# Optimization experiments

Hardware: AMD Instinct MI355X
Metric: run time of the kernel (lower is better)

The kernel has to match this reference:

```python
import jax, jax.numpy as jnp
import numpy as np

D = 1024
H = 16
HD = D // H
FF = 4 * D

def layer_norm(x, g, b, eps=1e-5):
    mu = jnp.mean(x, axis=-1, keepdims=True)
    var = jnp.var(x, axis=-1, keepdims=True)
    return (x - mu) * jax.lax.rsqrt(var + eps) * g + b

def setup_inputs() -> dict:
    key = jax.random.key(0)
    ks = jax.random.split(key, 8)
    s = 0.02
    return {
        "x": jax.random.normal(ks[0], (2, 2048, D), jnp.float32),
        "ln1_g": jnp.ones((D,), jnp.float32),
        "ln1_b": jnp.zeros((D,), jnp.float32),
        "w_qkv": jax.random.normal(ks[1], (3 * D, D), jnp.float32) * s,
        "b_qkv": jnp.zeros((3 * D,), jnp.float32),
        "w_proj": jax.random.normal(ks[2], (D, D), jnp.float32) * s,
        "b_proj": jnp.zeros((D,), jnp.float32),
        "ln2_g": jnp.ones((D,), jnp.float32),
        "ln2_b": jnp.zeros((D,), jnp.float32),
        "w_fc1": jax.random.normal(ks[3], (FF, D), jnp.float32) * s,
        "b_fc1": jnp.zeros((FF,), jnp.float32),
        "w_fc2": jax.random.normal(ks[4], (D, FF), jnp.float32) * s,
        "b_fc2": jnp.zeros((D,), jnp.float32),
    }

def reference(x, ln1_g, ln1_b, w_qkv, b_qkv, w_proj, b_proj,
              ln2_g, ln2_b, w_fc1, b_fc1, w_fc2, b_fc2):
    B, N, C = x.shape
    scale = HD ** -0.5
    # --- attention branch (pre-norm) ---
    h = layer_norm(x, ln1_g, ln1_b)
    qkv = h @ w_qkv.T + b_qkv                      # [B,N,3D]
    qkv = qkv.reshape(B, N, 3, H, HD).transpose(2, 0, 3, 1, 4)
    q, k, v = qkv[0], qkv[1], qkv[2]               # [B,H,N,HD]
    attn = jnp.einsum('bhnd,bhmd->bhnm', q, k) * scale
    attn = jax.nn.softmax(attn, axis=-1)
    o = jnp.einsum('bhnm,bhmd->bhnd', attn, v)     # [B,H,N,HD]
    o = o.transpose(0, 2, 1, 3).reshape(B, N, C)
    x = x + (o @ w_proj.T + b_proj)
    # --- FFN branch (pre-norm) ---
    h = layer_norm(x, ln2_g, ln2_b)
    h = jax.nn.gelu(h @ w_fc1.T + b_fc1, approximate=False)
    x = x + (h @ w_fc2.T + b_fc2)
    return x
```

## Files before the change

### kernel.cpp

```cpp
#include <hip/hip_runtime.h>

typedef __attribute__((ext_vector_type(8))) short short8;
typedef __attribute__((ext_vector_type(4))) float f32x4;

static __device__ __forceinline__ unsigned short f2bf(float f){
  unsigned u = __float_as_uint(f);
  u += 0x7FFF + ((u >> 16) & 1);
  return (unsigned short)(u >> 16);
}

static __device__ __forceinline__ f32x4 MF(short8 a, short8 b, f32x4 c){
  return __builtin_amdgcn_mfma_f32_16x16x32_bf16(a, b, c, 0, 0, 0);
}

#define GL16(g, l) __builtin_amdgcn_global_load_lds( \
    (const __attribute__((address_space(1))) void*)(g), \
    (__attribute__((address_space(3))) void*)(l), 16, 0, 0)

#define SBAR { __builtin_amdgcn_sched_barrier(0); __builtin_amdgcn_s_barrier(); __builtin_amdgcn_sched_barrier(0); }

__global__ __launch_bounds__(256) void cvt_all(
    const float* __restrict__ a0, const float* __restrict__ a1,
    const float* __restrict__ a2, const float* __restrict__ a3,
    unsigned short* __restrict__ o0, unsigned short* __restrict__ o1,
    unsigned short* __restrict__ o2, unsigned short* __restrict__ o3){
  int i = blockIdx.x * 256 + threadIdx.x;
  const float* src; unsigned short* dst; int off;
  if (i < 786432)       { src = a0; dst = o0; off = i; }
  else if (i < 1048576) { src = a1; dst = o1; off = i - 786432; }
  else if (i < 2097152) { src = a2; dst = o2; off = i - 1048576; }
  else                  { src = a3; dst = o3; off = i - 2097152; }
  float4 v = reinterpret_cast<const float4*>(src)[off];
  ushort4 o;
  o.x = f2bf(v.x); o.y = f2bf(v.y); o.z = f2bf(v.z); o.w = f2bf(v.w);
  reinterpret_cast<ushort4*>(dst)[off] = o;
}

__global__ __launch_bounds__(256) void ln_bf16(const float* __restrict__ x,
    const float* __restrict__ g, const float* __restrict__ b,
    unsigned short* __restrict__ out){
  int row = blockIdx.x, t = threadIdx.x;
  const float* xr = x + (size_t)row * 1024;
  float4 xv = reinterpret_cast<const float4*>(xr)[t];
  float s  = xv.x + xv.y + xv.z + xv.w;
  float sq = xv.x*xv.x + xv.y*xv.y + xv.z*xv.z + xv.w*xv.w;
  #pragma unroll
  for (int m = 32; m >= 1; m >>= 1){ s += __shfl_xor(s, m); sq += __shfl_xor(sq, m); }
  __shared__ float ss[4], ssq[4];
  int w = t >> 6, lane = t & 63;
  if (lane == 0){ ss[w] = s; ssq[w] = sq; }
  __syncthreads();
  s  = ss[0] + ss[1] + ss[2] + ss[3];
  sq = ssq[0] + ssq[1] + ssq[2] + ssq[3];
  float mu = s * (1.f/1024.f);
  float rs = rsqrtf(sq * (1.f/1024.f) - mu*mu + 1e-5f);
  float4 gv = reinterpret_cast<const float4*>(g)[t];
  float4 bv = reinterpret_cast<const float4*>(b)[t];
  ushort4 o;
  o.x = f2bf((xv.x - mu) * rs * gv.x + bv.x);
  o.y = f2bf((xv.y - mu) * rs * gv.y + bv.y);
  o.z = f2bf((xv.z - mu) * rs * gv.z + bv.z);
  o.w = f2bf((xv.w - mu) * rs * gv.w + bv.w);
  reinterpret_cast<ushort4*>(out + (size_t)row * 1024)[t] = o;
}

template<int EPI>
__global__ __launch_bounds__(512, 2) void gemm8p(
    const unsigned short* __restrict__ A,
    const unsigned short* __restrict__ B,
    const float* __restrict__ bias,
    void* __restrict__ C,
    int M, int N, int K)
{
  __shared__ __attribute__((aligned(16))) short As[2 * 256 * 64];
  __shared__ __attribute__((aligned(16))) short Bs[2 * 256 * 64];
  const int NT = K >> 6;
  int tid = threadIdx.x, lane = tid & 63, wave = tid >> 6;
  int wm = wave >> 2, wn = wave & 3;
  int l15 = lane & 15, hi = lane >> 4;
  int hi2 = hi ^ (((l15 >> 2) & 1) << 1);
  int bm = blockIdx.y * 256, bn = blockIdx.x * 256;
  int lr = lane >> 3;
  int sg8 = ((lane & 7) ^ ((lane >> 5) << 1)) * 8;
  int rb0 = wave * 16;

  f32x4 acc[8][4] = {};
  short8 aR[4][2], bA[2][2], bB[2][2];

  auto stage = [&](int T, int h){
    if (T >= NT) return;
    const unsigned short* src = (h < 2) ? (A + (size_t)(bm + ((h & 1) << 7)) * K)
                                        : (B + (size_t)(bn + ((h & 1) << 7)) * K);
    short* dst = ((h < 2) ? As : Bs) + ((T & 1) << 14) + ((h & 1) << 13);
    const unsigned short* s = src + (size_t)(rb0 + lr) * K + (T << 6) + sg8;
    GL16(s, dst + rb0 * 64);
    GL16(s + (size_t)8 * K, dst + (rb0 + 8) * 64);
  };
  auto LDA = [&](const short* Ab, int m, int kk){
    int R = wm * 128 + m * 16 + l15;
    return *(const short8*)(Ab + R * 64 + kk * 32 + hi2 * 8);
  };
  auto LDB = [&](const short* Bb, int n, int kk){
    int R = wn * 64 + n * 16 + l15;
    return *(const short8*)(Bb + R * 64 + kk * 32 + hi2 * 8);
  };

  stage(0, 0); stage(0, 1); stage(0, 2); stage(0, 3);
  stage(1, 0); stage(1, 1);
  asm volatile("s_waitcnt vmcnt(4)" ::: "memory");
  SBAR;

  for (int i = 0; i < (NT >> 1); ++i){
    int t0 = 2 * i, t1 = t0 + 1;
    const short* A0 = As;            const short* B0 = Bs;
    const short* A1 = As + 16384;    const short* B1 = Bs + 16384;
    #pragma unroll
    for (int m = 0; m < 4; m++){ aR[m][0] = LDA(A0, m, 0); aR[m][1] = LDA(A0, m, 1); }
    #pragma unroll
    for (int n = 0; n < 2; n++){ bA[n][0] = LDB(B0, n, 0); bA[n][1] = LDB(B0, n, 1); }
    __builtin_amdgcn_sched_barrier(0);
    stage(t1, 2);
    SBAR;
    __builtin_amdgcn_s_setprio(1);
    #pragma unroll
    for (int m = 0; m < 4; m++)
      #pragma unroll
      for (int n = 0; n < 2; n++)
        #pragma unroll
        for (int kk = 0; kk < 2; kk++) acc[m][n] = MF(aR[m][kk], bA[n][kk], acc[m][n]);
    __builtin_amdgcn_s_setprio(0);
    SBAR;
    #pragma unroll
    for (int n = 0; n < 2; n++){ bB[n][0] = LDB(B0, n + 2, 0); bB[n][1] = LDB(B0, n + 2, 1); }
    __builtin_amdgcn_sched_barrier(0);
    stage(t1, 3);
    SBAR;
    __builtin_amdgcn_s_setprio(1);
    #pragma unroll
    for (int m = 0; m < 4; m++)
      #pragma unroll
      for (int n = 0; n < 2; n++)
        #pragma unroll
        for (int kk = 0; kk < 2; kk++) acc[m][n + 2] = MF(aR[m][kk], bB[n][kk], acc[m][n + 2]);
    __builtin_amdgcn_s_setprio(0);
    SBAR;
    #pragma unroll
    for (int m = 0; m < 4; m++){ aR[m][0] = LDA(A0, m + 4, 0); aR[m][1] = LDA(A0, m + 4, 1); }
    __builtin_amdgcn_sched_barrier(0);
    stage(t0 + 2, 0);
    SBAR;
    __builtin_amdgcn_s_setprio(1);
    #pragma unroll
    for (int m = 0; m < 4; m++)
      #pragma unroll
      for (int n = 0; n < 2; n++)
        #pragma unroll
        for (int kk = 0; kk < 2; kk++) acc[m + 4][n] = MF(aR[m][kk], bA[n][kk], acc[m + 4][n]);
    __builtin_amdgcn_s_setprio(0);
    SBAR;
    stage(t0 + 2, 1);
    SBAR;
    __builtin_amdgcn_s_setprio(1);
    #pragma unroll
    for (int m = 0; m < 4; m++)
      #pragma unroll
      for (int n = 0; n < 2; n++)
        #pragma unroll
        for (int kk = 0; kk < 2; kk++) acc[m + 4][n + 2] = MF(aR[m][kk], bB[n][kk], acc[m + 4][n + 2]);
    __builtin_amdgcn_s_setprio(0);
    asm volatile("s_waitcnt vmcnt(4)" ::: "memory");
    SBAR;
    #pragma unroll
    for (int m = 0; m < 4; m++){ aR[m][0] = LDA(A1, m, 0); aR[m][1] = LDA(A1, m, 1); }
    #pragma unroll
    for (int n = 0; n < 2; n++){ bA[n][0] = LDB(B1, n, 0); bA[n][1] = LDB(B1, n, 1); }
    __builtin_amdgcn_sched_barrier(0);
    stage(t0 + 2, 2);
    SBAR;
    __builtin_amdgcn_s_setprio(1);
    #pragma unroll
    for (int m = 0; m < 4; m++)
      #pragma unroll
      for (int n = 0; n < 2; n++)
        #pragma unroll
        for (int kk = 0; kk < 2; kk++) acc[m][n] = MF(aR[m][kk], bA[n][kk], acc[m][n]);
    __builtin_amdgcn_s_setprio(0);
    SBAR;
    #pragma unroll
    for (int n = 0; n < 2; n++){ bB[n][0] = LDB(B1, n + 2, 0); bB[n][1] = LDB(B1, n + 2, 1); }
    __builtin_amdgcn_sched_barrier(0);
    stage(t0 + 2, 3);
    SBAR;
    __builtin_amdgcn_s_setprio(1);
    #pragma unroll
    for (int m = 0; m < 4; m++)
      #pragma unroll
      for (int n = 0; n < 2; n++)
        #pragma unroll
        for (int kk = 0; kk < 2; kk++) acc[m][n + 2] = MF(aR[m][kk], bB[n][kk], acc[m][n + 2]);
    __builtin_amdgcn_s_setprio(0);
    SBAR;
    #pragma unroll
    for (int m = 0; m < 4; m++){ aR[m][0] = LDA(A1, m + 4, 0); aR[m][1] = LDA(A1, m + 4, 1); }
    __builtin_amdgcn_sched_barrier(0);
    stage(t0 + 3, 0);
    SBAR;
    __builtin_amdgcn_s_setprio(1);
    #pragma unroll
    for (int m = 0; m < 4; m++)
      #pragma unroll
      for (int n = 0; n < 2; n++)
        #pragma unroll
        for (int kk = 0; kk < 2; kk++) acc[m + 4][n] = MF(aR[m][kk], bA[n][kk], acc[m + 4][n]);
    __builtin_amdgcn_s_setprio(0);
    SBAR;
    stage(t0 + 3, 1);
    SBAR;
    __builtin_amdgcn_s_setprio(1);
    #pragma unroll
    for (int m = 0; m < 4; m++)
      #pragma unroll
      for (int n = 0; n < 2; n++)
        #pragma unroll
        for (int kk = 0; kk < 2; kk++) acc[m + 4][n + 2] = MF(aR[m][kk], bB[n][kk], acc[m + 4][n + 2]);
    __builtin_amdgcn_s_setprio(0);
    asm volatile("s_waitcnt vmcnt(4)" ::: "memory");
    SBAR;
  }

  #pragma unroll
  for (int m = 0; m < 8; m++){
    int row = bm + wm * 128 + m * 16 + hi * 4;
    #pragma unroll
    for (int n = 0; n < 4; n++){
      int col = bn + wn * 64 + n * 16 + l15;
      float bv = bias[col];
      #pragma unroll
      for (int j = 0; j < 4; j++){
        float v = acc[m][n][j] + bv;
        if (EPI == 1) v = 0.5f * v * (1.f + erff(v * 0.70710678118654752f));
        ((unsigned short*)C)[(size_t)(row + j) * N + col] = f2bf(v);
      }
    }
  }
}

template<int TM, int EPI>
__global__ __launch_bounds__(256) void gemm_bt(
    const unsigned short* __restrict__ A,
    const unsigned short* __restrict__ B,
    const float* __restrict__ bias,
    const float* __restrict__ resid,
    void* __restrict__ C,
    int M, int N, int K)
{
  constexpr int MR = TM / 32;
  static_assert(TM / 32 + 4 == 6, "vmcnt literal assumes 6 loads per stage");
  __shared__ __attribute__((aligned(16))) short As[2][TM * 64];
  __shared__ __attribute__((aligned(16))) short Bs[2][128 * 64];
  int tid = threadIdx.x;
  int lane = tid & 63, wave = tid >> 6;
  int wm = wave >> 1, wn = wave & 1;
  int l15 = lane & 15, hi = lane >> 4;
  int bm = blockIdx.y * TM, bn = blockIdx.x * 128;
  int lr = lane >> 3, lseg = lane & 7;
  f32x4 acc[MR][4] = {};
  const int NT = K >> 6;
  auto stage = [&](int buf, int k0){
    #pragma unroll
    for (int j = 0; j < TM / 32; j++){
      int br = (wave * (TM / 32) + j) * 8;
      GL16(A + (size_t)(bm + br + lr) * K + k0 + lseg * 8, &As[buf][br * 64]);
    }
    #pragma unroll
    for (int j = 0; j < 4; j++){
      int br = (wave * 4 + j) * 8;
      GL16(B + (size_t)(bn + br + lr) * K + k0 + lseg * 8, &Bs[buf][br * 64]);
    }
  };
  stage(0, 0);
  for (int t = 0; t < NT; t++){
    int cur = t & 1;
    if (t + 1 < NT){
      stage(cur ^ 1, (t + 1) << 6);
      asm volatile("s_waitcnt vmcnt(6)" ::: "memory");
    } else {
      asm volatile("s_waitcnt vmcnt(0)" ::: "memory");
    }
    SBAR;
    #pragma unroll
    for (int kk = 0; kk < 64; kk += 32){
      short8 af[MR], bf[4];
      #pragma unroll
      for (int m = 0; m < MR; m++)
        af[m] = *reinterpret_cast<const short8*>(&As[cur][(wm*(TM/2) + m*16 + l15) * 64 + kk + hi*8]);
      #pragma unroll
      for (int n = 0; n < 4; n++)
        bf[n] = *reinterpret_cast<const short8*>(&Bs[cur][(wn*64 + n*16 + l15) * 64 + kk + hi*8]);
      #pragma unroll
      for (int m = 0; m < MR; m++)
        #pragma unroll
        for (int n = 0; n < 4; n++)
          acc[m][n] = __builtin_amdgcn_mfma_f32_16x16x32_bf16(af[m], bf[n], acc[m][n], 0, 0, 0);
    }
    SBAR;
  }
  #pragma unroll
  for (int m = 0; m < MR; m++){
    int row = bm + wm*(TM/2) + m*16 + hi*4;
    #pragma unroll
    for (int n = 0; n < 4; n++){
      int col = bn + wn*64 + n*16 + l15;
      float bv = bias[col];
      #pragma unroll
      for (int j = 0; j < 4; j++){
        float v = acc[m][n][j] + bv;
        int r = row + j;
        if (EPI == 1) v = 0.5f * v * (1.f + erff(v * 0.70710678118654752f));
        if (EPI == 2){
          ((float*)C)[(size_t)r * N + col] = v + resid[(size_t)r * N + col];
        } else {
          ((unsigned short*)C)[(size_t)r * N + col] = f2bf(v);
        }
      }
    }
  }
}

__global__ __launch_bounds__(512) void attn_fwd(const unsigned short* __restrict__ qkv,
                                                unsigned short* __restrict__ o){
  __shared__ __attribute__((aligned(16))) short K_lds[2][64*64];
  __shared__ __attribute__((aligned(16))) short V_lds[2][64*64];
  __shared__ __attribute__((aligned(16))) short P_lds[8][16*64];
  int tid = threadIdx.x, wave = tid >> 6, lane = tid & 63;
  int l15 = lane & 15, hi = lane >> 4, l7 = l15 & 7;
  int bid = blockIdx.x;
  int swz = (bid & 7) * 64 + (bid >> 3);
  int qt = swz & 15, bh = swz >> 4;
  int b = bh >> 4, h = bh & 15;
  const unsigned short* qbase = qkv + (size_t)b * 2048 * 3072 + h * 64;
  const unsigned short* kbase = qbase + 1024;
  const unsigned short* vbase = qbase + 2048;
  int qrow = qt * 128 + wave * 16 + l15;
  short8 qf0 = *(const short8*)(qbase + (size_t)qrow * 3072 + hi * 8);
  short8 qf1 = *(const short8*)(qbase + (size_t)qrow * 3072 + 32 + hi * 8);
  #pragma unroll
  for (int j = 0; j < 8; j++){
    float q0 = __uint_as_float((unsigned)(unsigned short)qf0[j] << 16) * 0.18033688f;
    float q1 = __uint_as_float((unsigned)(unsigned short)qf1[j] << 16) * 0.18033688f;
    qf0[j] = (short)f2bf(q0);
    qf1[j] = (short)f2bf(q1);
  }
  int krow = tid >> 3, kseg = tid & 7;
  int vt = tid - 256;
  int kp = vt & 31, ds8 = (vt >> 5) & 7;
  int vcg = kp >> 2, vwi = (2 * kp) & 7;
  float l_r = 0.f;
  f32x4 accO[4] = {};
  short* Pw = &P_lds[wave][0];

  {
    short8 kv = *(const short8*)(kbase + (size_t)krow * 3072 + kseg * 8);
    short8 vv0, vv1;
    if (vt >= 0){
      const unsigned short* vr = vbase + (size_t)(2 * kp) * 3072 + ds8 * 8;
      vv0 = *(const short8*)vr; vv1 = *(const short8*)(vr + 3072);
    }
    *(short8*)(&K_lds[0][krow * 64 + ((kseg ^ (krow & 7)) << 3)]) = kv;
    if (vt >= 0){
      unsigned* Vw = (unsigned*)&V_lds[0][0];
      #pragma unroll
      for (int j = 0; j < 8; j++){
        int d = ds8 * 8 + j;
        int sa = d * 64 + ((vcg ^ (d & 7)) << 3) + vwi;
        Vw[sa >> 1] = (unsigned)(unsigned short)vv0[j] | ((unsigned)(unsigned short)vv1[j] << 16);
      }
    }
    __syncthreads();
  }

  for (int t = 0; t < 32; t++){
    int cur = t & 1;
    const short* Kc = &K_lds[cur][0];
    const short* Vc = &V_lds[cur][0];
    short8 kv, vv0, vv1;
    if (t < 31){
      int kt = (t + 1) * 64;
      kv = *(const short8*)(kbase + (size_t)(kt + krow) * 3072 + kseg * 8);
      if (vt >= 0){
        const unsigned short* vr = vbase + (size_t)(kt + 2 * kp) * 3072 + ds8 * 8;
        vv0 = *(const short8*)vr; vv1 = *(const short8*)(vr + 3072);
      }
    }
    f32x4 sacc[4];
    __builtin_amdgcn_s_setprio(1);
    #pragma unroll
    for (int kb = 0; kb < 4; kb++){
      f32x4 s = {};
      short8 ka = *(const short8*)(Kc + (kb * 16 + l15) * 64 + ((hi ^ l7) << 3));
      s = __builtin_amdgcn_mfma_f32_16x16x32_bf16(ka, qf0, s, 0, 0, 0);
      short8 kb_ = *(const short8*)(Kc + (kb * 16 + l15) * 64 + (((4 + hi) ^ l7) << 3));
      s = __builtin_amdgcn_mfma_f32_16x16x32_bf16(kb_, qf1, s, 0, 0, 0);
      sacc[kb] = s;
    }
    __builtin_amdgcn_s_setprio(0);
    unsigned pu[8];
    #pragma unroll
    for (int kb = 0; kb < 4; kb++){
      float p0 = exp2f(sacc[kb][0]);
      float p1 = exp2f(sacc[kb][1]);
      float p2 = exp2f(sacc[kb][2]);
      float p3 = exp2f(sacc[kb][3]);
      l_r += (p0 + p1) + (p2 + p3);
      unsigned pka, pkb;
      asm("v_cvt_pk_bf16_f32 %0, %1, %2" : "=v"(pka) : "v"(p0), "v"(p1));
      asm("v_cvt_pk_bf16_f32 %0, %1, %2" : "=v"(pkb) : "v"(p2), "v"(p3));
      pu[kb * 2] = pka; pu[kb * 2 + 1] = pkb;
    }
    #pragma unroll
    for (int kb = 0; kb < 4; kb++){
      int sa = l15 * 64 + ((((kb << 1) | (hi >> 1)) ^ l7) << 3) + ((hi & 1) << 2);
      *(uint2*)(Pw + sa) = make_uint2(pu[kb * 2], pu[kb * 2 + 1]);
    }
    __builtin_amdgcn_s_setprio(1);
    #pragma unroll
    for (int kb2 = 0; kb2 < 2; kb2++){
      short8 pf = *(const short8*)(Pw + l15 * 64 + ((((kb2 << 2) | hi) ^ l7) << 3));
      #pragma unroll
      for (int db = 0; db < 4; db++){
        short8 vf = *(const short8*)(Vc + (db * 16 + l15) * 64 + ((((kb2 << 2) | hi) ^ l7) << 3));
        accO[db] = __builtin_amdgcn_mfma_f32_16x16x32_bf16(vf, pf, accO[db], 0, 0, 0);
      }
    }
    __builtin_amdgcn_s_setprio(0);
    if (t < 31){
      int nxt = cur ^ 1;
      *(short8*)(&K_lds[nxt][krow * 64 + ((kseg ^ (krow & 7)) << 3)]) = kv;
      if (vt >= 0){
        unsigned* Vw = (unsigned*)&V_lds[nxt][0];
        #pragma unroll
        for (int j = 0; j < 8; j++){
          int d = ds8 * 8 + j;
          int sa = d * 64 + ((vcg ^ (d & 7)) << 3) + vwi;
          Vw[sa >> 1] = (unsigned)(unsigned short)vv0[j] | ((unsigned)(unsigned short)vv1[j] << 16);
        }
      }
      __syncthreads();
    }
  }
  l_r += __shfl_xor(l_r, 16);
  l_r += __shfl_xor(l_r, 32);
  float inv = 1.f / l_r;
  unsigned short* ob = o + (size_t)(b * 2048 + qt * 128 + wave * 16 + l15) * 1024 + h * 64;
  #pragma unroll
  for (int db = 0; db < 4; db++){
    ushort4 w;
    w.x = f2bf(accO[db][0] * inv);
    w.y = f2bf(accO[db][1] * inv);
    w.z = f2bf(accO[db][2] * inv);
    w.w = f2bf(accO[db][3] * inv);
    *(ushort4*)(ob + db * 16 + hi * 4) = w;
  }
}

extern "C" void kernel_launch(void* const* d_in, const int* in_sizes, int n_in,
                              void* d_out, int out_size, void* d_ws, size_t ws_size,
                              hipStream_t stream){
  const float* x      = (const float*)d_in[0];
  const float* ln1_g  = (const float*)d_in[1];
  const float* ln1_b  = (const float*)d_in[2];
  const float* w_qkv  = (const float*)d_in[3];
  const float* b_qkv  = (const float*)d_in[4];
  const float* w_proj = (const float*)d_in[5];
  const float* b_proj = (const float*)d_in[6];
  const float* ln2_g  = (const float*)d_in[7];
  const float* ln2_b  = (const float*)d_in[8];
  const float* w_fc1  = (const float*)d_in[9];
  const float* b_fc1  = (const float*)d_in[10];
  const float* w_fc2  = (const float*)d_in[11];
  const float* b_fc2  = (const float*)d_in[12];
  float* out = (float*)d_out;
  char* ws = (char*)d_ws;
  const size_t MB = 1024 * 1024;
  unsigned short* h     = (unsigned short*)(ws);
  unsigned short* qkv   = (unsigned short*)(ws + 8*MB);
  unsigned short* ob    = (unsigned short*)(ws + 32*MB);
  float*          x1    = (float*)(ws + 40*MB);
  unsigned short* f     = (unsigned short*)(ws + 56*MB);
  unsigned short* wqkvb = (unsigned short*)(ws + 88*MB);
  unsigned short* wprojb= (unsigned short*)(ws + 94*MB);
  unsigned short* wfc1b = (unsigned short*)(ws + 96*MB);
  unsigned short* wfc2b = (unsigned short*)(ws + 104*MB);

  cvt_all<<<12288, 256, 0, stream>>>(w_qkv, w_proj, w_fc1, w_fc2,
                                     wqkvb, wprojb, wfc1b, wfc2b);

  ln_bf16<<<4096, 256, 0, stream>>>(x, ln1_g, ln1_b, h);
  gemm8p<0><<<dim3(12, 16), 512, 0, stream>>>(h, wqkvb, b_qkv, qkv, 4096, 3072, 1024);
  attn_fwd<<<512, 512, 0, stream>>>(qkv, ob);
  gemm_bt<64,2><<<dim3(8, 64), 256, 0, stream>>>(ob, wprojb, b_proj, x, x1, 4096, 1024, 1024);
  ln_bf16<<<4096, 256, 0, stream>>>(x1, ln2_g, ln2_b, h);
  gemm8p<1><<<dim3(16, 16), 512, 0, stream>>>(h, wfc1b, b_fc1, f, 4096, 4096, 1024);
  gemm_bt<64,2><<<dim3(8, 64), 256, 0, stream>>>(f, wfc2b, b_fc2, x1, out, 4096, 1024, 4096);
}
```

Measured before the change: 268.5 us.

## Use 8-wave blocks with XOR-swizzled LDS for residual-epilogue GEMMs

Replaces the 4-wave 64x128 tile GEMM used for the projection and FC2 layers with an 8-wave version. Each wave now computes a 32x32 subtile instead of 32x64, which halves the accumulator registers per wave and doubles the waves available to hide latency. It also XOR-swizzles the LDS layout on both the global-to-LDS copy and the fragment reads to avoid bank conflicts. In exchange, each wave issues more LDS reads per MFMA because it reuses fragments less, and the block needs more threads to synchronize at each barrier.

After: 244.0 us. 1.1x faster.

```diff
diff --git a/kernel.cpp b/kernel.cpp
--- a/kernel.cpp
+++ b/kernel.cpp
@@ -245,8 +245,8 @@
   }
 }
 
-template<int TM, int EPI>
-__global__ __launch_bounds__(256) void gemm_bt(
+template<int EPI>
+__global__ __launch_bounds__(512) void gemm_bt8(
     const unsigned short* __restrict__ A,
     const unsigned short* __restrict__ B,
     const float* __restrict__ bias,
@@ -254,69 +254,64 @@
     void* __restrict__ C,
     int M, int N, int K)
 {
-  constexpr int MR = TM / 32;
-  static_assert(TM / 32 + 4 == 6, "vmcnt literal assumes 6 loads per stage");
-  __shared__ __attribute__((aligned(16))) short As[2][TM * 64];
+  __shared__ __attribute__((aligned(16))) short As[2][64 * 64];
   __shared__ __attribute__((aligned(16))) short Bs[2][128 * 64];
   int tid = threadIdx.x;
   int lane = tid & 63, wave = tid >> 6;
-  int wm = wave >> 1, wn = wave & 1;
-  int l15 = lane & 15, hi = lane >> 4;
-  int bm = blockIdx.y * TM, bn = blockIdx.x * 128;
+  int wm = wave >> 2, wn = wave & 3;
+  int l15 = lane & 15, hi = lane >> 4, l7 = l15 & 7;
+  int bm = blockIdx.y * 64, bn = blockIdx.x * 128;
   int lr = lane >> 3, lseg = lane & 7;
-  f32x4 acc[MR][4] = {};
+  int sega = (lseg ^ lr) * 8;
+  f32x4 acc[2][2] = {};
   const int NT = K >> 6;
   auto stage = [&](int buf, int k0){
-    #pragma unroll
-    for (int j = 0; j < TM / 32; j++){
-      int br = (wave * (TM / 32) + j) * 8;
-      GL16(A + (size_t)(bm + br + lr) * K + k0 + lseg * 8, &As[buf][br * 64]);
-    }
-    #pragma unroll
-    for (int j = 0; j < 4; j++){
-      int br = (wave * 4 + j) * 8;
-      GL16(B + (size_t)(bn + br + lr) * K + k0 + lseg * 8, &Bs[buf][br * 64]);
-    }
+    GL16(A + (size_t)(bm + wave * 8 + lr) * K + k0 + sega, &As[buf][wave * 8 * 64]);
+    GL16(B + (size_t)(bn + wave * 16 + lr) * K + k0 + sega, &Bs[buf][wave * 16 * 64]);
+    GL16(B + (size_t)(bn + wave * 16 + 8 + lr) * K + k0 + sega, &Bs[buf][(wave * 16 + 8) * 64]);
   };
   stage(0, 0);
   for (int t = 0; t < NT; t++){
     int cur = t & 1;
     if (t + 1 < NT){
       stage(cur ^ 1, (t + 1) << 6);
-      asm volatile("s_waitcnt vmcnt(6)" ::: "memory");
+      asm volatile("s_waitcnt vmcnt(3)" ::: "memory");
     } else {
       asm volatile("s_waitcnt vmcnt(0)" ::: "memory");
     }
     SBAR;
     #pragma unroll
-    for (int kk = 0; kk < 64; kk += 32){
-      short8 af[MR], bf[4];
-      #pragma unroll
-      for (int m = 0; m < MR; m++)
-        af[m] = *reinterpret_cast<const short8*>(&As[cur][(wm*(TM/2) + m*16 + l15) * 64 + kk + hi*8]);
-      #pragma unroll
-      for (int n = 0; n < 4; n++)
-        bf[n] = *reinterpret_cast<const short8*>(&Bs[cur][(wn*64 + n*16 + l15) * 64 + kk + hi*8]);
-      #pragma unroll
-      for (int m = 0; m < MR; m++)
-        #pragma unroll
-        for (int n = 0; n < 4; n++)
-          acc[m][n] = __builtin_amdgcn_mfma_f32_16x16x32_bf16(af[m], bf[n], acc[m][n], 0, 0, 0);
+    for (int kk = 0; kk < 2; kk++){
+      short8 af[2], bf[2];
+      #pragma unroll
+      for (int m = 0; m < 2; m++){
+        int R = wm * 32 + m * 16 + l15;
+        af[m] = *(const short8*)(&As[cur][R * 64 + (((kk << 2) | hi) ^ l7) * 8]);
+      }
+      #pragma unroll
+      for (int n = 0; n < 2; n++){
+        int R = wn * 32 + n * 16 + l15;
+        bf[n] = *(const short8*)(&Bs[cur][R * 64 + (((kk << 2) | hi) ^ l7) * 8]);
+      }
+      #pragma unroll
+      for (int m = 0; m < 2; m++)
+        #pragma unroll
+        for (int n = 0; n < 2; n++)
+          acc[m][n] = MF(af[m], bf[n], acc[m][n]);
     }
     SBAR;
   }
   #pragma unroll
-  for (int m = 0; m < MR; m++){
-    int row = bm + wm*(TM/2) + m*16 + hi*4;
-    #pragma unroll
-    for (int n = 0; n < 4; n++){
-      int col = bn + wn*64 + n*16 + l15;
+  for (int m = 0; m < 2; m++){
+    int row = bm + wm * 32 + m * 16 + hi * 4;
+    #pragma unroll
+    for (int n = 0; n < 2; n++){
+      int col = bn + wn * 32 + n * 16 + l15;
       float bv = bias[col];
       #pragma unroll
       for (int j = 0; j < 4; j++){
         float v = acc[m][n][j] + bv;
         int r = row + j;
-        if (EPI == 1) v = 0.5f * v * (1.f + erff(v * 0.70710678118654752f));
         if (EPI == 2){
           ((float*)C)[(size_t)r * N + col] = v + resid[(size_t)r * N + col];
         } else {
@@ -498,8 +493,8 @@
   ln_bf16<<<4096, 256, 0, stream>>>(x, ln1_g, ln1_b, h);
   gemm8p<0><<<dim3(12, 16), 512, 0, stream>>>(h, wqkvb, b_qkv, qkv, 4096, 3072, 1024);
   attn_fwd<<<512, 512, 0, stream>>>(qkv, ob);
-  gemm_bt<64,2><<<dim3(8, 64), 256, 0, stream>>>(ob, wprojb, b_proj, x, x1, 4096, 1024, 1024);
+  gemm_bt8<2><<<dim3(8, 64), 512, 0, stream>>>(ob, wprojb, b_proj, x, x1, 4096, 1024, 1024);
   ln_bf16<<<4096, 256, 0, stream>>>(x1, ln2_g, ln2_b, h);
   gemm8p<1><<<dim3(16, 16), 512, 0, stream>>>(h, wfc1b, b_fc1, f, 4096, 4096, 1024);
-  gemm_bt<64,2><<<dim3(8, 64), 256, 0, stream>>>(f, wfc2b, b_fc2, x1, out, 4096, 1024, 4096);
-}
+  gemm_bt8<2><<<dim3(8, 64), 512, 0, stream>>>(f, wfc2b, b_fc2, x1, out, 4096, 1024, 4096);
+}
```
